# Performance work log

Hardware: AMD Instinct MI355X
Metric: run time of the kernel (lower is better)

The kernel has to match this reference:

```python
import jax, jax.numpy as jnp
import numpy as np
from jax import lax

N, H, W, C = 64, 256, 256, 16  # NHWC input
O, K = 16, 3                   # out_channels, kern_size


def setup_inputs() -> dict:
    key = jax.random.key(0)
    k_in, k_u, k_v, k_w = jax.random.split(key, 4)
    # glorot_normal std for shape [fan_in, fan_out]-ish 2D weights: sqrt(2/(a+b))
    u = jax.random.normal(k_u, (O, K), dtype=jnp.float32) * np.sqrt(2.0 / (O + K)).astype(np.float32)
    v = jax.random.normal(k_v, (O, K), dtype=jnp.float32) * np.sqrt(2.0 / (O + K)).astype(np.float32)
    w = jax.random.normal(k_w, (O, C), dtype=jnp.float32) * np.sqrt(2.0 / (O + C)).astype(np.float32)
    b = jnp.zeros((O,), dtype=jnp.float32)
    inputs = jax.random.normal(k_in, (N, H, W, C), dtype=jnp.float32)
    return {"inputs": inputs, "u": u, "v": v, "w": w, "b": b}


def reference(inputs, u, v, w, b):
    # CP low-rank kernel construction: kern[i,j,k,l] = v[l,i] * u[l,j] * w[l,k]
    # -> HWIO kernel of shape [K, K, C, O]
    kern = jnp.einsum('lj,lk,li->ijkl', u, w, v)
    out = lax.conv_general_dilated(
        inputs, kern,
        window_strides=(1, 1),
        padding='SAME',
        dimension_numbers=('NHWC', 'HWIO', 'NHWC'),
    )
    return jax.nn.relu(out + b)
```

## Files before the change

### kernel.cpp

```cpp
#include <hip/hip_runtime.h>
#include <hip/hip_bf16.h>

#define N_ 64
#define H_ 256
#define W_ 256
#define C_ 16
#define O_ 16
#define KS 3

#define TW 32
#define TH 16
#define HALO_W (TW + 2)
#define HALO_H (TH + 2)
#define PSTRIDE 20

__global__ __launch_bounds__(256, 3)
void sep_conv_kernel(const float* __restrict__ in,
                     const float* __restrict__ u,
                     const float* __restrict__ v,
                     const float* __restrict__ w,
                     const float* __restrict__ b,
                     float* __restrict__ out) {
    __shared__ float t_lds[HALO_H * HALO_W * PSTRIDE];

    const int tid = threadIdx.x;
    const int x0 = blockIdx.x * TW;
    const int y0 = blockIdx.y * TH;
    const int n  = blockIdx.z;

    const float* inbase = in + (size_t)n * H_ * W_ * C_;

    for (int p = tid; p < HALO_H * HALO_W; p += 256) {
        const int r = p / HALO_W;
        const int c = p - r * HALO_W;
        const int gy = y0 + r - 1;
        const int gx = x0 + c - 1;
        float tv[16];
        if ((unsigned)gy < (unsigned)H_ && (unsigned)gx < (unsigned)W_) {
            const float4* s4 = (const float4*)(inbase + ((size_t)gy * W_ + gx) * C_);
            const float4 a0 = s4[0];
            const float4 a1 = s4[1];
            const float4 a2 = s4[2];
            const float4 a3 = s4[3];
            float iv[16] = {a0.x, a0.y, a0.z, a0.w,
                            a1.x, a1.y, a1.z, a1.w,
                            a2.x, a2.y, a2.z, a2.w,
                            a3.x, a3.y, a3.z, a3.w};
            #pragma unroll
            for (int l = 0; l < 16; ++l) {
                float s = 0.f;
                #pragma unroll
                for (int k = 0; k < 16; ++k) {
                    s = fmaf(w[l * 16 + k], iv[k], s);
                }
                tv[l] = s;
            }
        } else {
            #pragma unroll
            for (int l = 0; l < 16; ++l) tv[l] = 0.f;
        }
        float4* d4 = (float4*)&t_lds[p * PSTRIDE];
        d4[0] = make_float4(tv[0],  tv[1],  tv[2],  tv[3]);
        d4[1] = make_float4(tv[4],  tv[5],  tv[6],  tv[7]);
        d4[2] = make_float4(tv[8],  tv[9],  tv[10], tv[11]);
        d4[3] = make_float4(tv[12], tv[13], tv[14], tv[15]);
    }
    __syncthreads();

    const int tx  = tid & (TW - 1);
    const int tyb = tid >> 5;
    #pragma unroll
    for (int pp = 0; pp < 2; ++pp) {
        const int ty = tyb + pp * 8;
        float acc[16];
        #pragma unroll
        for (int l = 0; l < 16; ++l) acc[l] = 0.f;

        #pragma unroll
        for (int i = 0; i < 3; ++i) {
            float h[16];
            #pragma unroll
            for (int l = 0; l < 16; ++l) h[l] = 0.f;
            #pragma unroll
            for (int j = 0; j < 3; ++j) {
                const float4* tp =
                    (const float4*)&t_lds[((ty + i) * HALO_W + (tx + j)) * PSTRIDE];
                const float4 a0 = tp[0];
                const float4 a1 = tp[1];
                const float4 a2 = tp[2];
                const float4 a3 = tp[3];
                const float tvv[16] = {a0.x, a0.y, a0.z, a0.w,
                                       a1.x, a1.y, a1.z, a1.w,
                                       a2.x, a2.y, a2.z, a2.w,
                                       a3.x, a3.y, a3.z, a3.w};
                #pragma unroll
                for (int l = 0; l < 16; ++l) {
                    h[l] = fmaf(u[l * 3 + j], tvv[l], h[l]);
                }
            }
            #pragma unroll
            for (int l = 0; l < 16; ++l) {
                acc[l] = fmaf(v[l * 3 + i], h[l], acc[l]);
            }
        }

        float r[16];
        #pragma unroll
        for (int l = 0; l < 16; ++l) {
            float val = acc[l] + b[l];
            r[l] = val > 0.f ? val : 0.f;
        }
        float4* o4 = (float4*)(out + (((size_t)n * H_ + (y0 + ty)) * W_ + (x0 + tx)) * C_);
        o4[0] = make_float4(r[0],  r[1],  r[2],  r[3]);
        o4[1] = make_float4(r[4],  r[5],  r[6],  r[7]);
        o4[2] = make_float4(r[8],  r[9],  r[10], r[11]);
        o4[3] = make_float4(r[12], r[13], r[14], r[15]);
    }
}

extern "C" void kernel_launch(void* const* d_in, const int* in_sizes, int n_in,
                              void* d_out, int out_size, void* d_ws, size_t ws_size,
                              hipStream_t stream) {
    const float* in = (const float*)d_in[0];
    const float* u  = (const float*)d_in[1];
    const float* v  = (const float*)d_in[2];
    const float* w  = (const float*)d_in[3];
    const float* b  = (const float*)d_in[4];
    float* out = (float*)d_out;

    dim3 grid(W_ / TW, H_ / TH, N_);
    dim3 block(256);
    sep_conv_kernel<<<grid, block, 0, stream>>>(in, u, v, w, b, out);
}
```

Before: 481.2 us.

## Halve tile height, raise occupancy, and issue both halo loads before compute

Reduces the output tile from 32x16 to 32x8 so each thread computes one output pixel, which shrinks LDS use and lets launch bounds request 5 blocks per CU instead of 3. The halo fill is restructured so each thread issues both of its global loads up front, then does the 1x1 channel mixing for each, giving more memory-level parallelism. The cost is more halo overhead, since 340 halo pixels now serve 256 outputs instead of 612 serving 512, so global reads and redundant 1x1 work go up. The tighter register cap may also risk spills.

```diff
diff --git a/kernel.cpp b/kernel.cpp
--- a/kernel.cpp
+++ b/kernel.cpp
@@ -6,22 +6,22 @@
 #define W_ 256
 #define C_ 16
 #define O_ 16
-#define KS 3
 
 #define TW 32
-#define TH 16
+#define TH 8
 #define HALO_W (TW + 2)
 #define HALO_H (TH + 2)
+#define NHALO (HALO_W * HALO_H)
 #define PSTRIDE 20
 
-__global__ __launch_bounds__(256, 3)
+__global__ __launch_bounds__(256, 5)
 void sep_conv_kernel(const float* __restrict__ in,
                      const float* __restrict__ u,
                      const float* __restrict__ v,
                      const float* __restrict__ w,
                      const float* __restrict__ b,
                      float* __restrict__ out) {
-    __shared__ float t_lds[HALO_H * HALO_W * PSTRIDE];
+    __shared__ float t_lds[NHALO * PSTRIDE];
 
     const int tid = threadIdx.x;
     const int x0 = blockIdx.x * TW;
@@ -30,36 +30,67 @@
 
     const float* inbase = in + (size_t)n * H_ * W_ * C_;
 
-    for (int p = tid; p < HALO_H * HALO_W; p += 256) {
-        const int r = p / HALO_W;
-        const int c = p - r * HALO_W;
-        const int gy = y0 + r - 1;
-        const int gx = x0 + c - 1;
+    const int p0 = tid;
+    const int p1 = tid + 256;
+    const bool has1 = (p1 < NHALO);
+
+    const int r0 = p0 / HALO_W, c0 = p0 - r0 * HALO_W;
+    const int r1 = p1 / HALO_W, c1 = p1 - r1 * HALO_W;
+    const int gy0 = y0 + r0 - 1, gx0 = x0 + c0 - 1;
+    const int gy1 = y0 + r1 - 1, gx1 = x0 + c1 - 1;
+    const bool in0 = (unsigned)gy0 < (unsigned)H_ && (unsigned)gx0 < (unsigned)W_;
+    const bool in1 = has1 && (unsigned)gy1 < (unsigned)H_ && (unsigned)gx1 < (unsigned)W_;
+
+    float4 A[4], B[4];
+    #pragma unroll
+    for (int q = 0; q < 4; ++q) A[q] = make_float4(0.f, 0.f, 0.f, 0.f);
+    #pragma unroll
+    for (int q = 0; q < 4; ++q) B[q] = make_float4(0.f, 0.f, 0.f, 0.f);
+
+    if (in0) {
+        const float4* s4 = (const float4*)(inbase + ((size_t)gy0 * W_ + gx0) * C_);
+        #pragma unroll
+        for (int q = 0; q < 4; ++q) A[q] = s4[q];
+    }
+    if (in1) {
+        const float4* s4 = (const float4*)(inbase + ((size_t)gy1 * W_ + gx1) * C_);
+        #pragma unroll
+        for (int q = 0; q < 4; ++q) B[q] = s4[q];
+    }
+
+    {
+        const float iv0[16] = {A[0].x, A[0].y, A[0].z, A[0].w,
+                               A[1].x, A[1].y, A[1].z, A[1].w,
+                               A[2].x, A[2].y, A[2].z, A[2].w,
+                               A[3].x, A[3].y, A[3].z, A[3].w};
         float tv[16];
-        if ((unsigned)gy < (unsigned)H_ && (unsigned)gx < (unsigned)W_) {
-            const float4* s4 = (const float4*)(inbase + ((size_t)gy * W_ + gx) * C_);
-            const float4 a0 = s4[0];
-            const float4 a1 = s4[1];
-            const float4 a2 = s4[2];
-            const float4 a3 = s4[3];
-            float iv[16] = {a0.x, a0.y, a0.z, a0.w,
-                            a1.x, a1.y, a1.z, a1.w,
-                            a2.x, a2.y, a2.z, a2.w,
-                            a3.x, a3.y, a3.z, a3.w};
+        #pragma unroll
+        for (int l = 0; l < 16; ++l) {
+            float s = 0.f;
             #pragma unroll
-            for (int l = 0; l < 16; ++l) {
-                float s = 0.f;
-                #pragma unroll
-                for (int k = 0; k < 16; ++k) {
-                    s = fmaf(w[l * 16 + k], iv[k], s);
-                }
-                tv[l] = s;
-            }
-        } else {
+            for (int k = 0; k < 16; ++k) s = fmaf(w[l * 16 + k], iv0[k], s);
+            tv[l] = s;
+        }
+        float4* d4 = (float4*)&t_lds[p0 * PSTRIDE];
+        d4[0] = make_float4(tv[0],  tv[1],  tv[2],  tv[3]);
+        d4[1] = make_float4(tv[4],  tv[5],  tv[6],  tv[7]);
+        d4[2] = make_float4(tv[8],  tv[9],  tv[10], tv[11]);
+        d4[3] = make_float4(tv[12], tv[13], tv[14], tv[15]);
+    }
+    if (has1) {
+        const float iv1[16] = {B[0].x, B[0].y, B[0].z, B[0].w,
+                               B[1].x, B[1].y, B[1].z, B[1].w,
+                               B[2].x, B[2].y, B[2].z, B[2].w,
+                               B[3].x, B[3].y, B[3].z, B[3].w};
+        float tv[16];
+        #pragma unroll
+        for (int l = 0; l < 16; ++l) {
+            float s = 0.f;
             #pragma unroll
-            for (int l = 0; l < 16; ++l) tv[l] = 0.f;
+            for (int k = 0; k < 16; ++k) s = fmaf(w[l * 16 + k], iv1[k], s);
+            tv[l] = s;
         }
-        float4* d4 = (float4*)&t_lds[p * PSTRIDE];
+        float4* d4 = (float4*)&t_lds[p1 * PSTRIDE];
         d4[0] = make_float4(tv[0],  tv[1],  tv[2],  tv[3]);
         d4[1] = make_float4(tv[4],  tv[5],  tv[6],  tv[7]);
         d4[2] = make_float4(tv[8],  tv[9],  tv[10], tv[11]);
@@ -67,55 +98,52 @@
     }
     __syncthreads();
 
-    const int tx  = tid & (TW - 1);
-    const int tyb = tid >> 5;
+    const int tx = tid & (TW - 1);
+    const int ty = tid >> 5;
+
+    float acc[16];
     #pragma unroll
-    for (int pp = 0; pp < 2; ++pp) {
-        const int ty = tyb + pp * 8;
-        float acc[16];
+    for (int l = 0; l < 16; ++l) acc[l] = 0.f;
+
+    #pragma unroll
+    for (int i = 0; i < 3; ++i) {
+        float h[16];
         #pragma unroll
-        for (int l = 0; l < 16; ++l) acc[l] = 0.f;
-
+        for (int l = 0; l < 16; ++l) h[l] = 0.f;
         #pragma unroll
-        for (int i = 0; i < 3; ++i) {
-            float h[16];
-            #pragma unroll
-            for (int l = 0; l < 16; ++l) h[l] = 0.f;
-            #pragma unroll
-            for (int j = 0; j < 3; ++j) {
-                const float4* tp =
-                    (const float4*)&t_lds[((ty + i) * HALO_W + (tx + j)) * PSTRIDE];
-                const float4 a0 = tp[0];
-                const float4 a1 = tp[1];
-                const float4 a2 = tp[2];
-                const float4 a3 = tp[3];
-                const float tvv[16] = {a0.x, a0.y, a0.z, a0.w,
-                                       a1.x, a1.y, a1.z, a1.w,
-                                       a2.x, a2.y, a2.z, a2.w,
-                                       a3.x, a3.y, a3.z, a3.w};
-                #pragma unroll
-                for (int l = 0; l < 16; ++l) {
-                    h[l] = fmaf(u[l * 3 + j], tvv[l], h[l]);
-                }
-            }
+        for (int j = 0; j < 3; ++j) {
+            const float4* tp =
+                (const float4*)&t_lds[((ty + i) * HALO_W + (tx + j)) * PSTRIDE];
+            const float4 a0 = tp[0];
+            const float4 a1 = tp[1];
+            const float4 a2 = tp[2];
+            const float4 a3 = tp[3];
+            const float tvv[16] = {a0.x, a0.y, a0.z, a0.w,
+                                   a1.x, a1.y, a1.z, a1.w,
+                                   a2.x, a2.y, a2.z, a2.w,
+                                   a3.x, a3.y, a3.z, a3.w};
             #pragma unroll
             for (int l = 0; l < 16; ++l) {
-                acc[l] = fmaf(v[l * 3 + i], h[l], acc[l]);
+                h[l] = fmaf(u[l * 3 + j], tvv[l], h[l]);
             }
         }
-
-        float r[16];
         #pragma unroll
         for (int l = 0; l < 16; ++l) {
-            float val = acc[l] + b[l];
-            r[l] = val > 0.f ? val : 0.f;
+            acc[l] = fmaf(v[l * 3 + i], h[l], acc[l]);
         }
-        float4* o4 = (float4*)(out + (((size_t)n * H_ + (y0 + ty)) * W_ + (x0 + tx)) * C_);
-        o4[0] = make_float4(r[0],  r[1],  r[2],  r[3]);
-        o4[1] = make_float4(r[4],  r[5],  r[6],  r[7]);
-        o4[2] = make_float4(r[8],  r[9],  r[10], r[11]);
-        o4[3] = make_float4(r[12], r[13], r[14], r[15]);
     }
+
+    float r[16];
+    #pragma unroll
+    for (int l = 0; l < 16; ++l) {
+        float val = acc[l] + b[l];
+        r[l] = val > 0.f ? val : 0.f;
+    }
+    float4* o4 = (float4*)(out + (((size_t)n * H_ + (y0 + ty)) * W_ + (x0 + tx)) * C_);
+    o4[0] = make_float4(r[0],  r[1],  r[2],  r[3]);
+    o4[1] = make_float4(r[4],  r[5],  r[6],  r[7]);
+    o4[2] = make_float4(r[8],  r[9],  r[10], r[11]);
+    o4[3] = make_float4(r[12], r[13], r[14], r[15]);
 }
 
 extern "C" void kernel_launch(void* const* d_in, const int* in_sizes, int n_in,
```

After: 463.5 us. 3.7% less time.
